# Optimization experiments

Hardware: AMD Instinct MI355X
Metric: run time of the kernel (lower is better)

Reference implementation:

```python
import jax, jax.numpy as jnp
import numpy as np

N = 30000        # nodes
E = 480000       # edges (before self-loops)
F_IN = 512       # input feature dim
HID = 64         # per-head hidden dim
HEADS = 4
WIDTH = HID * HEADS  # 256, concat heads
LAYERS = 3
NCLS = 40
NEG_SLOPE = 0.2


def setup_inputs() -> dict:
    key = jax.random.key(0)
    ks = jax.random.split(key, 16)
    def p(k, shape, scale=0.1):
        return jax.random.normal(k, shape, dtype=jnp.float32) * scale
    return {
        "x": jax.random.normal(ks[0], (N, F_IN), dtype=jnp.float32),
        "edge_index": jax.random.randint(ks[1], (2, E), 0, N, dtype=jnp.int32),
        # layer 1: F_IN -> HEADS*HID (concat)
        "W1": p(ks[2], (F_IN, WIDTH)), "as1": p(ks[3], (HEADS, HID)), "ad1": p(ks[4], (HEADS, HID)), "b1": p(ks[5], (WIDTH,)),
        # layer 2: WIDTH -> WIDTH
        "W2": p(ks[6], (WIDTH, WIDTH)), "as2": p(ks[7], (HEADS, HID)), "ad2": p(ks[8], (HEADS, HID)), "b2": p(ks[9], (WIDTH,)),
        # layer 3: WIDTH -> WIDTH
        "W3": p(ks[10], (WIDTH, WIDTH)), "as3": p(ks[11], (HEADS, HID)), "ad3": p(ks[12], (HEADS, HID)), "b3": p(ks[13], (WIDTH,)),
        # JK='cat' output head: WIDTH*LAYERS -> NCLS
        "Wo": p(ks[14], (WIDTH * LAYERS, NCLS)), "bo": p(ks[15], (NCLS,)),
    }


def gat_layer(x, Wm, a_src, a_dst, b, src, dst):
    # PyG GATConv (concat=True, eval mode): h = xW reshaped [N,H,C];
    # e_ij = leaky_relu(a_src.h_j + a_dst.h_i) for edge j->i, softmax over dst groups.
    n = x.shape[0]
    H, C = a_src.shape
    h = (x @ Wm).reshape(n, H, C)                      # [N,H,C]
    es = jnp.sum(h * a_src, axis=-1)                   # [N,H]
    ed = jnp.sum(h * a_dst, axis=-1)                   # [N,H]
    e = jax.nn.leaky_relu(es[src] + ed[dst], NEG_SLOPE)  # [Etot,H]
    m = jax.ops.segment_max(e, dst, num_segments=n)    # stable softmax per dst node
    w = jnp.exp(e - m[dst])
    den = jax.ops.segment_sum(w, dst, num_segments=n)
    alpha = w / den[dst]                               # [Etot,H]
    out = jax.ops.segment_sum(h[src] * alpha[:, :, None], dst, num_segments=n)  # [N,H,C]
    return out.reshape(n, H * C) + b


def reference(x, edge_index, W1, as1, ad1, b1, W2, as2, ad2, b2, W3, as3, ad3, b3, Wo, bo):
    # add self-loops (PyG GATConv default)
    loops = jnp.arange(N, dtype=edge_index.dtype)
    src = jnp.concatenate([edge_index[0], loops])
    dst = jnp.concatenate([edge_index[1], loops])
    # dropout is identity in eval mode
    h1 = jax.nn.relu(gat_layer(x, W1, as1, ad1, b1, src, dst))
    h2 = jax.nn.relu(gat_layer(h1, W2, as2, ad2, b2, src, dst))
    h3 = jax.nn.relu(gat_layer(h2, W3, as3, ad3, b3, src, dst))
    h = jnp.concatenate([h1, h2, h3], axis=-1)         # JK 'cat': [N, WIDTH*LAYERS]
    return h @ Wo + bo                                 # [N, NCLS]
```

## Files before the change

kernel.cpp:

```cpp
#include <hip/hip_runtime.h>

#define N_NODES 30000
#define N_EDGES 480000
#define ETOT    510000
#define F_IN    512
#define WIDTH   256
#define NCLS    40
#define KCAT    768
#define NPAD    48
#define TM      32
#define BROWS   272
#define HST     264

typedef __attribute__((ext_vector_type(8))) short short8;
typedef __attribute__((ext_vector_type(4))) float f32x4;

__device__ __forceinline__ unsigned short f2bf(float f){
  unsigned u = __float_as_uint(f);
  u += 0x7fffu + ((u >> 16) & 1u);
  return (unsigned short)(u >> 16);
}
__device__ __forceinline__ float b2f(unsigned short s){
  return __uint_as_float(((unsigned)s) << 16);
}

__device__ __forceinline__ void gload_lds16(const void* g, void* l){
  __builtin_amdgcn_global_load_lds(
      (const __attribute__((address_space(1))) unsigned int*)g,
      (__attribute__((address_space(3))) unsigned int*)l, 16, 0, 0);
}

__device__ __forceinline__ void av_body(const float* __restrict__ W,
                                        const float* __restrict__ a_s,
                                        const float* __restrict__ a_d,
                                        unsigned short* __restrict__ Bt, int K, int k){
  int tid = threadIdx.x;
  int h = tid >> 6, lane = tid & 63;
  float wv = W[(size_t)k * WIDTH + tid];
  float ps = wv * a_s[tid];
  float pd = wv * a_d[tid];
  #pragma unroll
  for (int off = 32; off; off >>= 1){
    ps += __shfl_down(ps, off, 64);
    pd += __shfl_down(pd, off, 64);
  }
  if (lane == 0){
    Bt[(size_t)(256 + h) * K + k] = f2bf(ps);
    Bt[(size_t)(260 + h) * K + k] = f2bf(pd);
  }
  if (tid < 8) Bt[(size_t)(264 + tid) * K + k] = 0;
}

#define PREP_GRID (118 + 512 + 256 + 256 + 144 + 512 + 256 + 256)

__global__ __launch_bounds__(256) void prep_kernel(
    const float* __restrict__ W1, const float* __restrict__ as1, const float* __restrict__ ad1,
    const float* __restrict__ W2, const float* __restrict__ as2, const float* __restrict__ ad2,
    const float* __restrict__ W3, const float* __restrict__ as3, const float* __restrict__ ad3,
    const float* __restrict__ Wo,
    unsigned short* __restrict__ Wt1, unsigned short* __restrict__ Wt2,
    unsigned short* __restrict__ Wt3, unsigned short* __restrict__ WoT,
    int* __restrict__ counts){
  int b = blockIdx.x, tid = threadIdx.x;
  if (b < 118){
    int i = b * 256 + tid;
    if (i < N_NODES) counts[i] = 0;
    return;
  }
  b -= 118;
  if (b < 512){
    int n = b >> 1, k = (b & 1) * 256 + tid;
    Wt1[(size_t)n * F_IN + k] = f2bf(W1[(size_t)k * WIDTH + n]);
    return;
  }
  b -= 512;
  if (b < 256){ Wt2[(size_t)b * WIDTH + tid] = f2bf(W2[(size_t)tid * WIDTH + b]); return; }
  b -= 256;
  if (b < 256){ Wt3[(size_t)b * WIDTH + tid] = f2bf(W3[(size_t)tid * WIDTH + b]); return; }
  b -= 256;
  if (b < 144){
    int i = b * 256 + tid;
    int c = i / KCAT, k = i - c * KCAT;
    WoT[i] = (c < NCLS) ? f2bf(Wo[(size_t)k * NCLS + c]) : (unsigned short)0;
    return;
  }
  b -= 144;
  if (b < 512){ av_body(W1, as1, ad1, Wt1, F_IN, b); return; }
  b -= 512;
  if (b < 256){ av_body(W2, as2, ad2, Wt2, WIDTH, b); return; }
  b -= 256;
  av_body(W3, as3, ad3, Wt3, WIDTH, b);
}

__global__ void hist_kernel(const int* __restrict__ ei, int* __restrict__ counts){
  int e = blockIdx.x * blockDim.x + threadIdx.x;
  if (e < ETOT){
    int d = (e < N_EDGES) ? ei[N_EDGES + e] : (e - N_EDGES);
    atomicAdd(&counts[d], 1);
  }
}

__global__ __launch_bounds__(1024) void scan_part_kernel(const int* __restrict__ counts,
                                                         int* __restrict__ offsets,
                                                         int* __restrict__ bsum, int n){
  __shared__ int wsum[16];
  int tid = threadIdx.x, lane = tid & 63, wid = tid >> 6;
  int i = blockIdx.x * 1024 + tid;
  int v = (i < n) ? counts[i] : 0;
  int x = v;
  #pragma unroll
  for (int off = 1; off < 64; off <<= 1){
    int t = __shfl_up(x, off, 64);
    if (lane >= off) x += t;
  }
  if (lane == 63) wsum[wid] = x;
  __syncthreads();
  if (wid == 0){
    int s = (lane < 16) ? wsum[lane] : 0;
    #pragma unroll
    for (int off = 1; off < 16; off <<= 1){
      int t = __shfl_up(s, off, 64);
      if (lane >= off) s += t;
    }
    if (lane < 16) wsum[lane] = s;
  }
  __syncthreads();
  int wp = (wid > 0) ? wsum[wid - 1] : 0;
  if (i < n) offsets[i] = x - v + wp;
  if (tid == 0) bsum[blockIdx.x] = wsum[15];
}

__global__ __launch_bounds__(64) void scan_bsum_kernel(int* __restrict__ bsum,
                                                       int* __restrict__ offsets,
                                                       int nb, int n){
  int lane = threadIdx.x;
  int v = (lane < nb) ? bsum[lane] : 0;
  int x = v;
  #pragma unroll
  for (int off = 1; off < 64; off <<= 1){
    int t = __shfl_up(x, off, 64);
    if (lane >= off) x += t;
  }
  if (lane < nb) bsum[lane] = x - v;
  if (lane == nb - 1) offsets[n] = x;
}

__global__ __launch_bounds__(1024) void scan_add_kernel(int* __restrict__ offsets,
                                                        int* __restrict__ cursor,
                                                        const int* __restrict__ bsum, int n){
  int i = blockIdx.x * 1024 + threadIdx.x;
  if (i < n){
    int o = offsets[i] + bsum[blockIdx.x];
    offsets[i] = o;
    cursor[i] = o;
  }
}

__global__ void scatter_kernel(const int* __restrict__ ei, int* __restrict__ cursor,
                               int* __restrict__ srcs){
  int e = blockIdx.x * blockDim.x + threadIdx.x;
  if (e < ETOT){
    int s, d;
    if (e < N_EDGES){ s = ei[e]; d = ei[N_EDGES + e]; }
    else { s = e - N_EDGES; d = s; }
    int pos = atomicAdd(&cursor[d], 1);
    srcs[pos] = s;
  }
}

template<int K, bool AF32>
__global__ __launch_bounds__(512, 4)
void gemm_bres_kernel(const void* __restrict__ Araw,
                      const unsigned short* __restrict__ Bt,
                      float* __restrict__ es,
                      float* __restrict__ ed,
                      unsigned short* __restrict__ hb,
                      int M){
  constexpr int KT = K / 32;
  constexpr int NP = K / 256;
  constexpr int KTP = KT / NP;
  constexpr int KE = KT / 8;
  constexpr int ROWB = K * 2;
  __shared__ unsigned short Abuf[TM * K];
  __shared__ unsigned short hstage[TM * HST];
  __shared__ float cmbE[8][TM][9];

  int tid = threadIdx.x;
  int lane = tid & 63, w = tid >> 6;
  int l15 = lane & 15, quad = lane >> 4;
  int c0 = w * 32;
  int r0 = blockIdx.x * TM;

  uint4 va[8];
  if constexpr (AF32){
    const char* xb = (const char*)Araw;
    #pragma unroll
    for (int i = 0; i < 8; ++i){
      int L32 = (i * 512 + tid) * 16;
      int row = L32 >> 11;
      int colb = L32 & 2047;
      int grow = r0 + row; if (grow > M - 1) grow = M - 1;
      va[i] = *(const uint4*)(xb + (size_t)grow * 2048 + colb);
    }
  } else {
    const char* Ab = (const char*)Araw;
    #pragma unroll
    for (int c = 0; c < 2; ++c){
      int L = (c * 512 + tid) * 16;
      int row = L / ROWB;
      int colb = L % ROWB;
      int grow = r0 + row; if (grow > M - 1) grow = M - 1;
      gload_lds16(Ab + (size_t)grow * ROWB + (colb ^ ((row & 7) << 4)),
                  (char*)Abuf + L);
    }
  }

  short8 Bfe[KE];
  #pragma unroll
  for (int i = 0; i < KE; ++i){
    int kt = w * KE + i;
    Bfe[i] = *(const short8*)(Bt + (size_t)(256 + l15) * K + kt*32 + quad*8);
  }

  if constexpr (AF32){
    #pragma unroll
    for (int i = 0; i < 8; ++i){
      int ob = (i * 512 + tid) * 8;
      int row = ob >> 10;
      unsigned u0 = (unsigned)f2bf(__uint_as_float(va[i].x)) |
                    ((unsigned)f2bf(__uint_as_float(va[i].y)) << 16);
      unsigned u1 = (unsigned)f2bf(__uint_as_float(va[i].z)) |
                    ((unsigned)f2bf(__uint_as_float(va[i].w)) << 16);
      uint2 uv; uv.x = u0; uv.y = u1;
      *(uint2*)((char*)Abuf + (ob ^ ((row & 7) << 4))) = uv;
    }
  }
  __syncthreads();

  f32x4 acc[2][2];
  f32x4 eacc[2];
  #pragma unroll
  for (int s = 0; s < 2; ++s){
    acc[s][0] = (f32x4){0.f,0.f,0.f,0.f};
    acc[s][1] = (f32x4){0.f,0.f,0.f,0.f};
    eacc[s]   = (f32x4){0.f,0.f,0.f,0.f};
  }

  #pragma unroll 1
  for (int p = 0; p < NP; ++p){
    short8 Bf[KTP][2];
    #pragma unroll
    for (int kt2 = 0; kt2 < KTP; ++kt2){
      #pragma unroll
      for (int ct = 0; ct < 2; ++ct){
        Bf[kt2][ct] = *(const short8*)(Bt + (size_t)(c0 + ct*16 + l15) * K
                                          + (p*KTP + kt2)*32 + quad*8);
      }
    }
    __builtin_amdgcn_sched_barrier(0);
    #pragma unroll
    for (int s = 0; s < 2; ++s){
      int row = s * 16 + l15;
      int swzus = (row & 7) << 3;
      const unsigned short* base = Abuf + row * K;
      #pragma unroll
      for (int kt2 = 0; kt2 < KTP; ++kt2){
        int kofs = (p*KTP + kt2)*32 + quad*8;
        short8 af = *(const short8*)(base + (kofs ^ swzus));
        acc[s][0] = __builtin_amdgcn_mfma_f32_16x16x32_bf16(af, Bf[kt2][0], acc[s][0], 0, 0, 0);
        acc[s][1] = __builtin_amdgcn_mfma_f32_16x16x32_bf16(af, Bf[kt2][1], acc[s][1], 0, 0, 0);
      }
    }
  }

  #pragma unroll
  for (int s = 0; s < 2; ++s){
    int row = s * 16 + l15;
    int swzus = (row & 7) << 3;
    const unsigned short* base = Abuf + row * K;
    #pragma unroll
    for (int i = 0; i < KE; ++i){
      int kt = w * KE + i;
      short8 af = *(const short8*)(base + ((kt*32 + quad*8) ^ swzus));
      eacc[s] = __builtin_amdgcn_mfma_f32_16x16x32_bf16(af, Bfe[i], eacc[s], 0, 0, 0);
    }
  }

  #pragma unroll
  for (int s = 0; s < 2; ++s){
    #pragma unroll
    for (int r = 0; r < 4; ++r){
      int row = s * 16 + quad * 4 + r;
      hstage[row * HST + c0 + l15]      = f2bf(acc[s][0][r]);
      hstage[row * HST + c0 + 16 + l15] = f2bf(acc[s][1][r]);
      if (l15 < 8) cmbE[w][row][l15] = eacc[s][r];
    }
  }
  __syncthreads();

  #pragma unroll
  for (int p2 = 0; p2 < 2; ++p2){
    int us = (p2 * 512 + tid) * 8;
    int row = us >> 8, col = us & 255;
    if (r0 + row < M){
      uint4 v = *(const uint4*)(&hstage[row * HST + col]);
      *(uint4*)(hb + (size_t)(r0 + row) * WIDTH + col) = v;
    }
  }
  if (tid < 256){
    int row = tid >> 3, j = tid & 7;
    if (r0 + row < M){
      float v = 0.f;
      #pragma unroll
      for (int ww = 0; ww < 8; ++ww) v += cmbE[ww][row][j];
      if (j < 4) es[(size_t)(r0 + row) * 4 + j] = v;
      else       ed[(size_t)(r0 + row) * 4 + (j - 4)] = v;
    }
  }
}

__global__ __launch_bounds__(256) void agg_kernel(const int* __restrict__ offsets,
                                                  const int* __restrict__ srcs,
                                                  const float* __restrict__ es,
                                                  const float* __restrict__ ed,
                                                  const unsigned short* __restrict__ hb,
                                                  const float* __restrict__ bias,
                                                  unsigned short* __restrict__ hout){
  __shared__ float eLds[8][64][4];
  __shared__ int   sLds[8][64];
  int wid = threadIdx.x >> 6;
  int lane = threadIdx.x & 63;
  int half = lane >> 5, l32 = lane & 31;
  int slot = wid * 2 + half;
  int n = blockIdx.x * 8 + slot;
  int base = offsets[n];
  int deg = offsets[n + 1] - base;
  float4 edv = *(const float4*)(ed + (size_t)n * 4);

  float m0 = -1e30f, m1 = -1e30f, m2 = -1e30f, m3 = -1e30f;
  for (int i = l32; i < deg; i += 32){
    int s = srcs[base + i];
    float4 ev = *(const float4*)(es + (size_t)s * 4);
    float e0 = ev.x + edv.x, e1 = ev.y + edv.y, e2 = ev.z + edv.z, e3 = ev.w + edv.w;
    e0 = e0 > 0.f ? e0 : 0.2f * e0;
    e1 = e1 > 0.f ? e1 : 0.2f * e1;
    e2 = e2 > 0.f ? e2 : 0.2f * e2;
    e3 = e3 > 0.f ? e3 : 0.2f * e3;
    if (i < 64){
      sLds[slot][i] = s;
      *(float4*)(&eLds[slot][i][0]) = (float4){e0, e1, e2, e3};
    }
    m0 = fmaxf(m0, e0); m1 = fmaxf(m1, e1); m2 = fmaxf(m2, e2); m3 = fmaxf(m3, e3);
  }
  #pragma unroll
  for (int off = 1; off < 32; off <<= 1){
    m0 = fmaxf(m0, __shfl_xor(m0, off, 64));
    m1 = fmaxf(m1, __shfl_xor(m1, off, 64));
    m2 = fmaxf(m2, __shfl_xor(m2, off, 64));
    m3 = fmaxf(m3, __shfl_xor(m3, off, 64));
  }
  int head = l32 >> 3;
  float mh  = (head == 0) ? m0 : (head == 1) ? m1 : (head == 2) ? m2 : m3;
  float edh = (head == 0) ? edv.x : (head == 1) ? edv.y : (head == 2) ? edv.z : edv.w;

  float2 a0 = {0.f,0.f}, a1 = {0.f,0.f}, a2 = {0.f,0.f}, a3 = {0.f,0.f};
  float den = 0.f;
  const unsigned short* hcol = hb + 8 * l32;
  for (int i = 0; i < deg; i += 8){
    int sidx[8]; float wgt[8];
    #pragma unroll
    for (int u = 0; u < 8; ++u){
      int idx = i + u;
      bool v = idx < deg;
      float le; int s;
      if (idx < 64 || !v){
        int ic = v ? idx : 0;
        if (ic >= 64) ic = 0;
        s  = sLds[slot][ic];
        le = eLds[slot][ic][head];
      } else {
        s = srcs[base + idx];
        float e = es[(size_t)s * 4 + head] + edh;
        le = e > 0.f ? e : 0.2f * e;
      }
      sidx[u] = s;
      wgt[u] = v ? __expf(le - mh) : 0.f;
    }
    uint4 hv[8];
    #pragma unroll
    for (int u = 0; u < 8; ++u)
      hv[u] = *(const uint4*)(hcol + (size_t)sidx[u] * WIDTH);
    #pragma unroll
    for (int u = 0; u < 8; ++u){
      float wu = wgt[u];
      den += wu;
      a0.x += wu * __uint_as_float(hv[u].x << 16);
      a0.y += wu * __uint_as_float(hv[u].x & 0xffff0000u);
      a1.x += wu * __uint_as_float(hv[u].y << 16);
      a1.y += wu * __uint_as_float(hv[u].y & 0xffff0000u);
      a2.x += wu * __uint_as_float(hv[u].z << 16);
      a2.y += wu * __uint_as_float(hv[u].z & 0xffff0000u);
      a3.x += wu * __uint_as_float(hv[u].w << 16);
      a3.y += wu * __uint_as_float(hv[u].w & 0xffff0000u);
    }
  }
  float inv = 1.0f / den;
  const float* bp = bias + 8 * l32;
  float4 bv0 = *(const float4*)(bp);
  float4 bv1 = *(const float4*)(bp + 4);
  float o0 = fmaxf(a0.x * inv + bv0.x, 0.f);
  float o1 = fmaxf(a0.y * inv + bv0.y, 0.f);
  float o2 = fmaxf(a1.x * inv + bv0.z, 0.f);
  float o3 = fmaxf(a1.y * inv + bv0.w, 0.f);
  float o4 = fmaxf(a2.x * inv + bv1.x, 0.f);
  float o5 = fmaxf(a2.y * inv + bv1.y, 0.f);
  float o6 = fmaxf(a3.x * inv + bv1.z, 0.f);
  float o7 = fmaxf(a3.y * inv + bv1.w, 0.f);
  uint4 o;
  o.x = (unsigned)f2bf(o0) | ((unsigned)f2bf(o1) << 16);
  o.y = (unsigned)f2bf(o2) | ((unsigned)f2bf(o3) << 16);
  o.z = (unsigned)f2bf(o4) | ((unsigned)f2bf(o5) << 16);
  o.w = (unsigned)f2bf(o6) | ((unsigned)f2bf(o7) << 16);
  *(uint4*)(hout + (size_t)n * WIDTH + 8 * l32) = o;
}

__global__ __launch_bounds__(256) void out_gemm_kernel(const unsigned short* __restrict__ h1,
                                                       const unsigned short* __restrict__ h2,
                                                       const unsigned short* __restrict__ h3,
                                                       const unsigned short* __restrict__ WoT,
                                                       const float* __restrict__ bo,
                                                       float* __restrict__ out){
  int tid = threadIdx.x, lane = tid & 63, wid = tid >> 6;
  int l15 = lane & 15, quad = lane >> 4;
  int m0 = blockIdx.x * 64 + 16 * wid;

  f32x4 acc[3];
  #pragma unroll
  for (int t = 0; t < 3; ++t) acc[t] = (f32x4){0.f, 0.f, 0.f, 0.f};

  int arow = m0 + l15; if (arow >= N_NODES) arow = N_NODES - 1;

  #pragma unroll
  for (int part = 0; part < 3; ++part){
    const unsigned short* hp = (part == 0) ? h1 : (part == 1) ? h2 : h3;
    const unsigned short* ap = hp + (size_t)arow * WIDTH;
    #pragma unroll
    for (int k0 = 0; k0 < WIDTH; k0 += 32){
      short8 af = *(const short8*)(ap + k0 + quad * 8);
      int kk = part * WIDTH + k0;
      #pragma unroll
      for (int t = 0; t < 3; ++t){
        short8 bf = *(const short8*)(WoT + (size_t)(16 * t + l15) * KCAT + kk + quad * 8);
        acc[t] = __builtin_amdgcn_mfma_f32_16x16x32_bf16(af, bf, acc[t], 0, 0, 0);
      }
    }
  }

  int r0 = m0 + quad * 4;
  #pragma unroll
  for (int t = 0; t < 3; ++t){
    int col = 16 * t + l15;
    if (col < NCLS){
      float bc = bo[col];
      #pragma unroll
      for (int r = 0; r < 4; ++r){
        int grow = r0 + r;
        if (grow < N_NODES) out[(size_t)grow * NCLS + col] = acc[t][r] + bc;
      }
    }
  }
}

static inline size_t align256(size_t x){ return (x + 255) & ~(size_t)255; }

extern "C" void kernel_launch(void* const* d_in, const int* in_sizes, int n_in,
                              void* d_out, int out_size, void* d_ws, size_t ws_size,
                              hipStream_t stream) {
  const float* x   = (const float*)d_in[0];
  const int*   ei  = (const int*)  d_in[1];
  const float* W1  = (const float*)d_in[2];
  const float* as1 = (const float*)d_in[3];
  const float* ad1 = (const float*)d_in[4];
  const float* b1  = (const float*)d_in[5];
  const float* W2  = (const float*)d_in[6];
  const float* as2 = (const float*)d_in[7];
  const float* ad2 = (const float*)d_in[8];
  const float* b2  = (const float*)d_in[9];
  const float* W3  = (const float*)d_in[10];
  const float* as3 = (const float*)d_in[11];
  const float* ad3 = (const float*)d_in[12];
  const float* b3  = (const float*)d_in[13];
  const float* Wo  = (const float*)d_in[14];
  const float* bo  = (const float*)d_in[15];
  float* out = (float*)d_out;

  char* p = (char*)d_ws;
  auto take = [&](size_t bytes) -> char* { char* cur = p; p += align256(bytes); return cur; };

  unsigned short* Wt1   = (unsigned short*)take((size_t)BROWS * F_IN * 2);
  unsigned short* Wt2   = (unsigned short*)take((size_t)BROWS * WIDTH * 2);
  unsigned short* Wt3   = (unsigned short*)take((size_t)BROWS * WIDTH * 2);
  unsigned short* WoT   = (unsigned short*)take((size_t)NPAD * KCAT * 2);
  unsigned short* hs    = (unsigned short*)take((size_t)N_NODES * WIDTH * 2);
  float*          es    = (float*)take((size_t)N_NODES * 4 * 4);
  float*          ed    = (float*)take((size_t)N_NODES * 4 * 4);
  unsigned short* h1b   = (unsigned short*)take((size_t)N_NODES * WIDTH * 2);
  unsigned short* h2b   = (unsigned short*)take((size_t)N_NODES * WIDTH * 2);
  unsigned short* h3b   = (unsigned short*)take((size_t)N_NODES * WIDTH * 2);
  int*            counts  = (int*)take((size_t)N_NODES * 4);
  int*            offsets = (int*)take((size_t)(N_NODES + 1) * 4);
  int*            cursor  = (int*)take((size_t)N_NODES * 4);
  int*            srcs    = (int*)take((size_t)ETOT * 4);
  int*            bsum    = (int*)take((size_t)64 * 4);

  prep_kernel<<<PREP_GRID, 256, 0, stream>>>(W1, as1, ad1, W2, as2, ad2,
                                             W3, as3, ad3, Wo,
                                             Wt1, Wt2, Wt3, WoT, counts);

  const int nb = (N_NODES + 1023) / 1024;
  hist_kernel<<<(ETOT + 255) / 256, 256, 0, stream>>>(ei, counts);
  scan_part_kernel<<<nb, 1024, 0, stream>>>(counts, offsets, bsum, N_NODES);
  scan_bsum_kernel<<<1, 64, 0, stream>>>(bsum, offsets, nb, N_NODES);
  scan_add_kernel<<<nb, 1024, 0, stream>>>(offsets, cursor, bsum, N_NODES);
  scatter_kernel<<<(ETOT + 255) / 256, 256, 0, stream>>>(ei, cursor, srcs);

  const int ntiles = (N_NODES + TM - 1) / TM;
  const int agg_grid = N_NODES / 8;
  const int out_grid = (N_NODES + 63) / 64;

  gemm_bres_kernel<F_IN, true><<<ntiles, 512, 0, stream>>>(x, Wt1, es, ed, hs, N_NODES);
  agg_kernel<<<agg_grid, 256, 0, stream>>>(offsets, srcs, es, ed, hs, b1, h1b);
  gemm_bres_kernel<WIDTH, false><<<ntiles, 512, 0, stream>>>(h1b, Wt2, es, ed, hs, N_NODES);
  agg_kernel<<<agg_grid, 256, 0, stream>>>(offsets, srcs, es, ed, hs, b2, h2b);
  gemm_bres_kernel<WIDTH, false><<<ntiles, 512, 0, stream>>>(h2b, Wt3, es, ed, hs, N_NODES);
  agg_kernel<<<agg_grid, 256, 0, stream>>>(offsets, srcs, es, ed, hs, b3, h3b);

  out_gemm_kernel<<<out_grid, 256, 0, stream>>>(h1b, h2b, h3b, WoT, bo, out);
}
```

Measured before the change: 385.0 us.

## Double GEMM row tile, stream K in 256-wide chunks, fuse edge scatter

The projection GEMM tile grows from 32 to 64 rows. The A operand is now staged through LDS in 256-column chunks instead of a full K row, and the output staging buffer reuses the A buffer with a swizzle. This raises B-fragment reuse per block and lowers LDS footprint per row. The CSR scatter kernel is folded into the first GEMM launch as extra blocks, removing one launch and letting the scatter overlap the GEMM. The risks are fewer blocks (about 469 tiles) and extra syncs per K chunk.

New measurement: 387.3 us. No clear change (+0.6%).

```diff
diff --git a/kernel.cpp b/kernel.cpp
--- a/kernel.cpp
+++ b/kernel.cpp
@@ -8,9 +8,8 @@
 #define NCLS    40
 #define KCAT    768
 #define NPAD    48
-#define TM      32
+#define TM      64
 #define BROWS   272
-#define HST     264
 
 typedef __attribute__((ext_vector_type(8))) short short8;
 typedef __attribute__((ext_vector_type(4))) float f32x4;
@@ -156,18 +155,6 @@
   }
 }
 
-__global__ void scatter_kernel(const int* __restrict__ ei, int* __restrict__ cursor,
-                               int* __restrict__ srcs){
-  int e = blockIdx.x * blockDim.x + threadIdx.x;
-  if (e < ETOT){
-    int s, d;
-    if (e < N_EDGES){ s = ei[e]; d = ei[N_EDGES + e]; }
-    else { s = e - N_EDGES; d = s; }
-    int pos = atomicAdd(&cursor[d], 1);
-    srcs[pos] = s;
-  }
-}
-
 template<int K, bool AF32>
 __global__ __launch_bounds__(512, 4)
 void gemm_bres_kernel(const void* __restrict__ Araw,
@@ -175,46 +162,35 @@
                       float* __restrict__ es,
                       float* __restrict__ ed,
                       unsigned short* __restrict__ hb,
-                      int M){
+                      int M, int ngb,
+                      const int* __restrict__ ei,
+                      int* __restrict__ cursor,
+                      int* __restrict__ srcs){
   constexpr int KT = K / 32;
   constexpr int NP = K / 256;
-  constexpr int KTP = KT / NP;
   constexpr int KE = KT / 8;
-  constexpr int ROWB = K * 2;
-  __shared__ unsigned short Abuf[TM * K];
-  __shared__ unsigned short hstage[TM * HST];
+  __shared__ unsigned short Abuf[TM * 256];
   __shared__ float cmbE[8][TM][9];
 
   int tid = threadIdx.x;
+
+  if ((int)blockIdx.x >= ngb){
+    int e = ((int)blockIdx.x - ngb) * 512 + tid;
+    if (e < ETOT){
+      int s, d;
+      if (e < N_EDGES){ s = ei[e]; d = ei[N_EDGES + e]; }
+      else { s = e - N_EDGES; d = s; }
+      int pos = atomicAdd(&cursor[d], 1);
+      srcs[pos] = s;
+    }
+    return;
+  }
+
   int lane = tid & 63, w = tid >> 6;
   int l15 = lane & 15, quad = lane >> 4;
   int c0 = w * 32;
   int r0 = blockIdx.x * TM;
 
-  uint4 va[8];
-  if constexpr (AF32){
-    const char* xb = (const char*)Araw;
-    #pragma unroll
-    for (int i = 0; i < 8; ++i){
-      int L32 = (i * 512 + tid) * 16;
-      int row = L32 >> 11;
-      int colb = L32 & 2047;
-      int grow = r0 + row; if (grow > M - 1) grow = M - 1;
-      va[i] = *(const uint4*)(xb + (size_t)grow * 2048 + colb);
-    }
-  } else {
-    const char* Ab = (const char*)Araw;
-    #pragma unroll
-    for (int c = 0; c < 2; ++c){
-      int L = (c * 512 + tid) * 16;
-      int row = L / ROWB;
-      int colb = L % ROWB;
-      int grow = r0 + row; if (grow > M - 1) grow = M - 1;
-      gload_lds16(Ab + (size_t)grow * ROWB + (colb ^ ((row & 7) << 4)),
-                  (char*)Abuf + L);
-    }
-  }
-
   short8 Bfe[KE];
   #pragma unroll
   for (int i = 0; i < KE; ++i){
@@ -222,25 +198,10 @@
     Bfe[i] = *(const short8*)(Bt + (size_t)(256 + l15) * K + kt*32 + quad*8);
   }
 
-  if constexpr (AF32){
-    #pragma unroll
-    for (int i = 0; i < 8; ++i){
-      int ob = (i * 512 + tid) * 8;
-      int row = ob >> 10;
-      unsigned u0 = (unsigned)f2bf(__uint_as_float(va[i].x)) |
-                    ((unsigned)f2bf(__uint_as_float(va[i].y)) << 16);
-      unsigned u1 = (unsigned)f2bf(__uint_as_float(va[i].z)) |
-                    ((unsigned)f2bf(__uint_as_float(va[i].w)) << 16);
-      uint2 uv; uv.x = u0; uv.y = u1;
-      *(uint2*)((char*)Abuf + (ob ^ ((row & 7) << 4))) = uv;
-    }
-  }
-  __syncthreads();
-
-  f32x4 acc[2][2];
-  f32x4 eacc[2];
-  #pragma unroll
-  for (int s = 0; s < 2; ++s){
+  f32x4 acc[4][2];
+  f32x4 eacc[4];
+  #pragma unroll
+  for (int s = 0; s < 4; ++s){
     acc[s][0] = (f32x4){0.f,0.f,0.f,0.f};
     acc[s][1] = (f32x4){0.f,0.f,0.f,0.f};
     eacc[s]   = (f32x4){0.f,0.f,0.f,0.f};
@@ -248,73 +209,120 @@
 
   #pragma unroll 1
   for (int p = 0; p < NP; ++p){
-    short8 Bf[KTP][2];
-    #pragma unroll
-    for (int kt2 = 0; kt2 < KTP; ++kt2){
+    if (p) __syncthreads();
+    if constexpr (AF32){
+      const char* xb = (const char*)Araw;
+      uint4 va[8];
+      #pragma unroll
+      for (int i = 0; i < 8; ++i){
+        int L32 = (i * 512 + tid) * 16;
+        int row = L32 >> 10;
+        int colb = L32 & 1023;
+        int grow = r0 + row; if (grow > M - 1) grow = M - 1;
+        va[i] = *(const uint4*)(xb + (size_t)grow * (K*4) + p*1024 + colb);
+      }
+      #pragma unroll
+      for (int i = 0; i < 8; ++i){
+        int ob = (i * 512 + tid) * 8;
+        int row = ob >> 9;
+        unsigned u0 = (unsigned)f2bf(__uint_as_float(va[i].x)) |
+                      ((unsigned)f2bf(__uint_as_float(va[i].y)) << 16);
+        unsigned u1 = (unsigned)f2bf(__uint_as_float(va[i].z)) |
+                      ((unsigned)f2bf(__uint_as_float(va[i].w)) << 16);
+        uint2 uv; uv.x = u0; uv.y = u1;
+        *(uint2*)((char*)Abuf + (ob ^ ((row & 7) << 4))) = uv;
+      }
+    } else {
+      const char* Ab = (const char*)Araw;
+      #pragma unroll
+      for (int c = 0; c < 4; ++c){
+        int L = (c * 512 + tid) * 16;
+        int row = L >> 9;
+        int colb = L & 511;
+        int grow = r0 + row; if (grow > M - 1) grow = M - 1;
+        gload_lds16(Ab + (size_t)grow * (K*2) + p*512 + (colb ^ ((row & 7) << 4)),
+                    (char*)Abuf + L);
+      }
+    }
+    __syncthreads();
+
+    short8 Bf[8][2];
+    #pragma unroll
+    for (int kt2 = 0; kt2 < 8; ++kt2){
       #pragma unroll
       for (int ct = 0; ct < 2; ++ct){
         Bf[kt2][ct] = *(const short8*)(Bt + (size_t)(c0 + ct*16 + l15) * K
-                                          + (p*KTP + kt2)*32 + quad*8);
+                                          + (p*8 + kt2)*32 + quad*8);
       }
     }
     __builtin_amdgcn_sched_barrier(0);
-    #pragma unroll
-    for (int s = 0; s < 2; ++s){
+
+    #pragma unroll
+    for (int s = 0; s < 4; ++s){
       int row = s * 16 + l15;
       int swzus = (row & 7) << 3;
-      const unsigned short* base = Abuf + row * K;
-      #pragma unroll
-      for (int kt2 = 0; kt2 < KTP; ++kt2){
-        int kofs = (p*KTP + kt2)*32 + quad*8;
-        short8 af = *(const short8*)(base + (kofs ^ swzus));
+      const unsigned short* base = Abuf + row * 256;
+      #pragma unroll
+      for (int kt2 = 0; kt2 < 8; ++kt2){
+        short8 af = *(const short8*)(base + ((kt2*32 + quad*8) ^ swzus));
         acc[s][0] = __builtin_amdgcn_mfma_f32_16x16x32_bf16(af, Bf[kt2][0], acc[s][0], 0, 0, 0);
         acc[s][1] = __builtin_amdgcn_mfma_f32_16x16x32_bf16(af, Bf[kt2][1], acc[s][1], 0, 0, 0);
       }
     }
-  }
-
-  #pragma unroll
-  for (int s = 0; s < 2; ++s){
-    int row = s * 16 + l15;
-    int swzus = (row & 7) << 3;
-    const unsigned short* base = Abuf + row * K;
     #pragma unroll
     for (int i = 0; i < KE; ++i){
       int kt = w * KE + i;
-      short8 af = *(const short8*)(base + ((kt*32 + quad*8) ^ swzus));
-      eacc[s] = __builtin_amdgcn_mfma_f32_16x16x32_bf16(af, Bfe[i], eacc[s], 0, 0, 0);
-    }
-  }
-
-  #pragma unroll
-  for (int s = 0; s < 2; ++s){
+      if (kt >= p*8 && kt < p*8 + 8){
+        int kt2 = kt - p*8;
+        #pragma unroll
+        for (int s = 0; s < 4; ++s){
+          int row = s * 16 + l15;
+          int swzus = (row & 7) << 3;
+          const unsigned short* base = Abuf + row * 256;
+          short8 af = *(const short8*)(base + ((kt2*32 + quad*8) ^ swzus));
+          eacc[s] = __builtin_amdgcn_mfma_f32_16x16x32_bf16(af, Bfe[i], eacc[s], 0, 0, 0);
+        }
+      }
+    }
+  }
+
+  __syncthreads();
+  #pragma unroll
+  for (int s = 0; s < 4; ++s){
     #pragma unroll
     for (int r = 0; r < 4; ++r){
       int row = s * 16 + quad * 4 + r;
-      hstage[row * HST + c0 + l15]      = f2bf(acc[s][0][r]);
-      hstage[row * HST + c0 + 16 + l15] = f2bf(acc[s][1][r]);
+      int swz = (row & 7) << 4;
+      #pragma unroll
+      for (int ct = 0; ct < 2; ++ct){
+        int colb = (c0 + ct * 16 + l15) * 2;
+        *(unsigned short*)((char*)Abuf + ((row * 512 + colb) ^ swz))
+            = f2bf(acc[s][ct][r]);
+      }
       if (l15 < 8) cmbE[w][row][l15] = eacc[s][r];
     }
   }
   __syncthreads();
 
   #pragma unroll
-  for (int p2 = 0; p2 < 2; ++p2){
-    int us = (p2 * 512 + tid) * 8;
+  for (int c = 0; c < 4; ++c){
+    int us = (c * 512 + tid) * 8;
     int row = us >> 8, col = us & 255;
-    if (r0 + row < M){
-      uint4 v = *(const uint4*)(&hstage[row * HST + col]);
-      *(uint4*)(hb + (size_t)(r0 + row) * WIDTH + col) = v;
-    }
-  }
-  if (tid < 256){
+    int grow = r0 + row;
+    if (grow < M){
+      uint4 v = *(const uint4*)((const char*)Abuf + ((row * 512 + col * 2) ^ ((row & 7) << 4)));
+      *(uint4*)(hb + (size_t)grow * WIDTH + col) = v;
+    }
+  }
+  {
     int row = tid >> 3, j = tid & 7;
-    if (r0 + row < M){
+    int grow = r0 + row;
+    if (grow < M){
       float v = 0.f;
       #pragma unroll
       for (int ww = 0; ww < 8; ++ww) v += cmbE[ww][row][j];
-      if (j < 4) es[(size_t)(r0 + row) * 4 + j] = v;
-      else       ed[(size_t)(r0 + row) * 4 + (j - 4)] = v;
+      if (j < 4) es[(size_t)grow * 4 + j] = v;
+      else       ed[(size_t)grow * 4 + (j - 4)] = v;
     }
   }
 }
@@ -522,17 +530,20 @@
   scan_part_kernel<<<nb, 1024, 0, stream>>>(counts, offsets, bsum, N_NODES);
   scan_bsum_kernel<<<1, 64, 0, stream>>>(bsum, offsets, nb, N_NODES);
   scan_add_kernel<<<nb, 1024, 0, stream>>>(offsets, cursor, bsum, N_NODES);
-  scatter_kernel<<<(ETOT + 255) / 256, 256, 0, stream>>>(ei, cursor, srcs);
 
   const int ntiles = (N_NODES + TM - 1) / TM;
+  const int nscat  = (ETOT + 511) / 512;
   const int agg_grid = N_NODES / 8;
   const int out_grid = (N_NODES + 63) / 64;
 
-  gemm_bres_kernel<F_IN, true><<<ntiles, 512, 0, stream>>>(x, Wt1, es, ed, hs, N_NODES);
+  gemm_bres_kernel<F_IN, true><<<ntiles + nscat, 512, 0, stream>>>(
+      x, Wt1, es, ed, hs, N_NODES, ntiles, ei, cursor, srcs);
   agg_kernel<<<agg_grid, 256, 0, stream>>>(offsets, srcs, es, ed, hs, b1, h1b);
-  gemm_bres_kernel<WIDTH, false><<<ntiles, 512, 0, stream>>>(h1b, Wt2, es, ed, hs, N_NODES);
+  gemm_bres_kernel<WIDTH, false><<<ntiles, 512, 0, stream>>>(
+      h1b, Wt2, es, ed, hs, N_NODES, ntiles, ei, cursor, srcs);
   agg_kernel<<<agg_grid, 256, 0, stream>>>(offsets, srcs, es, ed, hs, b2, h2b);
-  gemm_bres_kernel<WIDTH, false><<<ntiles, 512, 0, stream>>>(h2b, Wt3, es, ed, hs, N_NODES);
+  gemm_bres_kernel<WIDTH, false><<<ntiles, 512, 0, stream>>>(
+      h2b, Wt3, es, ed, hs, N_NODES, ntiles, ei, cursor, srcs);
   agg_kernel<<<agg_grid, 256, 0, stream>>>(offsets, srcs, es, ed, hs, b3, h3b);
 
   out_gemm_kernel<<<out_grid, 256, 0, stream>>>(h1b, h2b, h3b, WoT, bo, out);
```
